# Kernel optimization log

Hardware: AMD Instinct MI355X
Metric: run time of the kernel (lower is better)

## Reference

```python
import jax, jax.numpy as jnp
import numpy as np

K = 5            # kernel_size
MAX_ORIENT = 8
MAX_LEVEL = 4
D = (K - 1) // 2  # pad amount = 2


def setup_inputs() -> dict:
    key = jax.random.key(0)
    k1, k2, k3 = jax.random.split(key, 3)
    x = jax.random.normal(k1, (32, 1, 512, 512), dtype=jnp.float32)
    fwd_f = jax.random.normal(k2, (MAX_ORIENT, 1, K, K), dtype=jnp.float32)
    fwd_f = fwd_f.at[0, 0].set(jnp.ones((K, K), dtype=jnp.float32))  # per __init__
    inv_f = jax.random.normal(k3, (MAX_ORIENT, 1, K, K), dtype=jnp.float32)
    return {"x": x, "forward_filters": fwd_f, "inverse_filters": inv_f}


def _pad_for_tconv(p):
    # faithful port of padding_for_transpose_conv (static python ints)
    ip, op = 0, 0
    if p > 0:
        op = p
    elif p < 0:
        a = -p
        if a % 2 == 0:
            ip = a // 2
        else:
            op = 1
            ip = (a + 1) // 2
    return ip, op


def _conv2d(x, w, stride, pad):
    # torch F.pad(x, (d,d,d,d)) then conv2d(stride) == conv with symmetric padding
    return jax.lax.conv_general_dilated(
        x, w, window_strides=(stride, stride),
        padding=((pad, pad), (pad, pad)),
        dimension_numbers=("NCHW", "OIHW", "NCHW"))


def _conv_transpose2d(x, w, stride, pad, out_pad):
    # torch conv_transpose2d, weight layout (in_ch, out_ch, kH, kW).
    # Equivalent direct conv: flip kernel spatially, swap I/O axes,
    # lhs_dilation=stride, padding lo=k-1-p, hi=k-1-p+output_padding.
    k = w.shape[2]
    w2 = jnp.transpose(jnp.flip(w, (2, 3)), (1, 0, 2, 3))  # OIHW (1,8,5,5)
    padding = tuple((k - 1 - p, k - 1 - p + op) for p, op in zip(pad, out_pad))
    return jax.lax.conv_general_dilated(
        x, w2, window_strides=(1, 1), padding=padding,
        lhs_dilation=(stride, stride),
        dimension_numbers=("NCHW", "OIHW", "NCHW"))


def _forward_transform(x, fwd_f):
    result = [None] * (MAX_LEVEL + 1)
    vimg = x
    level = MAX_LEVEL
    res = None
    while level > 0 and vimg.shape[2] > 1 and vimg.shape[3] > 1:
        res = _conv2d(vimg, fwd_f, 2, D)   # (B, 8, ceil(H/2)+?, ...)
        result[level] = res
        vimg = res[:, :1]                  # lowpass band feeds next level
        level -= 1
    result[0] = res[:, :1]
    return result


def _inverse_transform(coeffs, inp_dim, inv_f):
    rec = coeffs[0]
    for level in range(1, MAX_LEVEL + 1):
        cur = np.array(coeffs[level].shape[2:])
        target = np.array(inp_dim) if level == MAX_LEVEL else np.array(coeffs[level + 1].shape[2:])
        pc = target - 2 * (cur - 1) - K
        ip0, op0 = _pad_for_tconv(int(pc[0]))
        ip1, op1 = _pad_for_tconv(int(pc[1]))
        full = jnp.concatenate([rec, coeffs[level][:, 1:]], axis=1)  # (B,8,h,w)
        rec = _conv_transpose2d(full, inv_f, 2, (ip0, ip1), (op0, op1))
    return rec


def reference(x, forward_filters, inverse_filters):
    coeffs = _forward_transform(x, forward_filters)
    return _inverse_transform(coeffs, x.shape[2:], inverse_filters)
```

## Files before the change

### kernel.cpp

```cpp
#include <hip/hip_runtime.h>

#define NORIENT 8

__device__ __forceinline__ unsigned xcd_swz(unsigned bid, unsigned nwg) {
    unsigned chunk = nwg >> 3;
    return (nwg & 7u) ? bid : (bid & 7u) * chunk + (bid >> 3);
}

__global__ void fwd_conv_kernel(const float* __restrict__ in, long in_img_stride,
                                const float* __restrict__ filt,
                                float* __restrict__ out,
                                int H, int W, int OH, int OW, int N) {
    int OH2 = OH >> 1, OW2 = OW >> 1;
    unsigned sb = xcd_swz(blockIdx.x, gridDim.x);
    long idx = (long)sb * blockDim.x + threadIdx.x;
    long total = (long)N * OH2 * OW2;
    if (idx >= total) return;
    int ox2 = (int)(idx % OW2);
    long t = idx / OW2;
    int oy2 = (int)(t % OH2);
    int n = (int)(t / OH2);

    const float* __restrict__ ip = in + (long)n * in_img_stride;
    int y0 = 4 * oy2 - 2, x0 = 4 * ox2 - 2;

    float patch[7][7];
#pragma unroll
    for (int i = 0; i < 7; ++i) {
        int y = y0 + i;
        bool vy = (y >= 0) & (y < H);
        const float* rowp = ip + (long)(vy ? y : 0) * W;
#pragma unroll
        for (int j = 0; j < 7; ++j) {
            int x = x0 + j;
            bool vx = (x >= 0) & (x < W);
            float v = rowp[vx ? x : 0];
            patch[i][j] = (vy & vx) ? v : 0.f;
        }
    }

    long cs = (long)OH * OW;
    long ob0 = (long)n * NORIENT * cs + (long)(2 * oy2) * OW + 2 * ox2;
#pragma unroll
    for (int c = 0; c < NORIENT; ++c) {
        const float* __restrict__ F = filt + c * 25;
        float a00 = 0.f, a01 = 0.f, a10 = 0.f, a11 = 0.f;
#pragma unroll
        for (int i = 0; i < 5; ++i) {
#pragma unroll
            for (int j = 0; j < 5; ++j) {
                float wv = F[i * 5 + j];
                a00 = fmaf(patch[i][j],         wv, a00);
                a01 = fmaf(patch[i][j + 2],     wv, a01);
                a10 = fmaf(patch[i + 2][j],     wv, a10);
                a11 = fmaf(patch[i + 2][j + 2], wv, a11);
            }
        }
        long ob = ob0 + (long)c * cs;
        *(float2*)&out[ob]      = make_float2(a00, a01);
        *(float2*)&out[ob + OW] = make_float2(a10, a11);
    }
}

__global__ void inv_tconv_kernel(const float* __restrict__ rec, long rec_img_stride,
                                 const float* __restrict__ coef,
                                 const float* __restrict__ filt,
                                 float* __restrict__ out,
                                 int h, int w, int N) {
    int h2 = h >> 1, w2 = w >> 1;
    unsigned sb = xcd_swz(blockIdx.x, gridDim.x);
    long idx = (long)sb * blockDim.x + threadIdx.x;
    long total = (long)N * h2 * w2;
    if (idx >= total) return;
    int b0 = (int)(idx % w2);
    long t = idx / w2;
    int a0 = (int)(t % h2);
    int n = (int)(t / h2);

    const float* __restrict__ rp = rec + (long)n * rec_img_stride;
    const float* __restrict__ cp = coef + (long)n * (long)NORIENT * h * w;
    int cs = h * w;

    bool fmv = a0 > 0, fpv = a0 < h2 - 1;
    bool um = b0 > 0, up = b0 < w2 - 1;
    float fm = fmv ? 1.f : 0.f, fp_ = fpv ? 1.f : 0.f;
    int r0 = (fmv ? 2 * a0 - 1 : 0) * w;
    int r1 = (2 * a0) * w;
    int r2 = (2 * a0 + 1) * w;
    int r3 = (fpv ? 2 * a0 + 2 : 2 * a0 + 1) * w;
    int cL = um ? 2 * b0 - 2 : 0;
    int cM = 2 * b0;
    int cR = up ? 2 * b0 + 2 : 0;

    float acc[2][2][2][2];
#pragma unroll
    for (int i = 0; i < 2; ++i)
#pragma unroll
        for (int j = 0; j < 2; ++j)
#pragma unroll
            for (int k = 0; k < 2; ++k)
#pragma unroll
                for (int l = 0; l < 2; ++l) acc[i][j][k][l] = 0.f;

    auto do_channel = [&](const float* __restrict__ src, const float* __restrict__ F) {
        float P[4][4];
        const int ro[4] = {r0, r1, r2, r3};
        const float rm[4] = {fm, 1.f, 1.f, fp_};
#pragma unroll
        for (int r = 0; r < 4; ++r) {
            const float* base = src + ro[r];
            float2 L = *(const float2*)(base + cL);
            float2 M = *(const float2*)(base + cM);
            float2 R = *(const float2*)(base + cR);
            float mask = rm[r];
            P[r][0] = (um ? L.y : 0.f) * mask;
            P[r][1] = M.x * mask;
            P[r][2] = M.y * mask;
            P[r][3] = (up ? R.x : 0.f) * mask;
        }
#pragma unroll
        for (int a = 0; a < 3; ++a) {
#pragma unroll
            for (int b = 0; b < 3; ++b) {
                float w00 = F[(4 - 2 * a) * 5 + (4 - 2 * b)];
                float w01 = (b >= 1) ? F[(4 - 2 * a) * 5 + (5 - 2 * b)] : 0.f;
                float w10 = (a >= 1) ? F[(5 - 2 * a) * 5 + (4 - 2 * b)] : 0.f;
                float w11 = (a >= 1 && b >= 1) ? F[(5 - 2 * a) * 5 + (5 - 2 * b)] : 0.f;
#pragma unroll
                for (int sr = 0; sr < 2; ++sr) {
#pragma unroll
                    for (int sc = 0; sc < 2; ++sc) {
                        float pv = P[sr + a][sc + b];
                        acc[sr][sc][0][0] = fmaf(pv, w00, acc[sr][sc][0][0]);
                        if (b >= 1) acc[sr][sc][0][1] = fmaf(pv, w01, acc[sr][sc][0][1]);
                        if (a >= 1) acc[sr][sc][1][0] = fmaf(pv, w10, acc[sr][sc][1][0]);
                        if (a >= 1 && b >= 1)
                                    acc[sr][sc][1][1] = fmaf(pv, w11, acc[sr][sc][1][1]);
                    }
                }
            }
        }
    };

    do_channel(rp, filt);
#pragma unroll
    for (int c = 1; c < NORIENT; ++c)
        do_channel(cp + (long)c * cs, filt + c * 25);

    int OW = w << 1;
    long ob = (long)n * 4 * (long)cs + (long)(4 * a0) * OW + 4 * b0;
    *(float4*)(out + ob)          = make_float4(acc[0][0][0][0], acc[0][0][0][1],
                                                acc[0][1][0][0], acc[0][1][0][1]);
    *(float4*)(out + ob + OW)     = make_float4(acc[0][0][1][0], acc[0][0][1][1],
                                                acc[0][1][1][0], acc[0][1][1][1]);
    *(float4*)(out + ob + 2 * OW) = make_float4(acc[1][0][0][0], acc[1][0][0][1],
                                                acc[1][1][0][0], acc[1][1][0][1]);
    *(float4*)(out + ob + 3 * OW) = make_float4(acc[1][0][1][0], acc[1][0][1][1],
                                                acc[1][1][1][0], acc[1][1][1][1]);
}

extern "C" void kernel_launch(void* const* d_in, const int* in_sizes, int n_in,
                              void* d_out, int out_size, void* d_ws, size_t ws_size,
                              hipStream_t stream) {
    const float* x     = (const float*)d_in[0];
    const float* fwd_f = (const float*)d_in[1];
    const float* inv_f = (const float*)d_in[2];
    float* out = (float*)d_out;
    float* ws  = (float*)d_ws;

    const int N = 32;

    float* l4 = ws;
    float* l3 = l4 + 16777216;
    float* l2 = l3 + 4194304;
    float* l1 = l2 + 1048576;
    float* r1 = l1 + 262144;
    float* r2 = r1 + 131072;
    float* r3 = r2 + 524288;

    dim3 blk(256);
    auto nblocks = [](long total) { return dim3((unsigned)((total + 255) / 256)); };

    fwd_conv_kernel<<<nblocks(32L * 128 * 128), blk, 0, stream>>>(
        x, 512L * 512, fwd_f, l4, 512, 512, 256, 256, N);
    fwd_conv_kernel<<<nblocks(32L * 64 * 64), blk, 0, stream>>>(
        l4, 8L * 256 * 256, fwd_f, l3, 256, 256, 128, 128, N);
    fwd_conv_kernel<<<nblocks(32L * 32 * 32), blk, 0, stream>>>(
        l3, 8L * 128 * 128, fwd_f, l2, 128, 128, 64, 64, N);
    fwd_conv_kernel<<<nblocks(32L * 16 * 16), blk, 0, stream>>>(
        l2, 8L * 64 * 64, fwd_f, l1, 64, 64, 32, 32, N);

    inv_tconv_kernel<<<nblocks(32L * 16 * 16), blk, 0, stream>>>(
        l1, 8L * 32 * 32, l1, inv_f, r1, 32, 32, N);
    inv_tconv_kernel<<<nblocks(32L * 32 * 32), blk, 0, stream>>>(
        r1, 64L * 64, l2, inv_f, r2, 64, 64, N);
    inv_tconv_kernel<<<nblocks(32L * 64 * 64), blk, 0, stream>>>(
        r2, 128L * 128, l3, inv_f, r3, 128, 128, N);
    inv_tconv_kernel<<<nblocks(32L * 128 * 128), blk, 0, stream>>>(
        r3, 256L * 256, l4, inv_f, out, 256, 256, N);
}
```

Before: 112.8 us.

## Compute 2x4 output tile per thread in forward conv with float4 row loads

```diff
diff --git a/kernel.cpp b/kernel.cpp
--- a/kernel.cpp
+++ b/kernel.cpp
@@ -11,54 +11,74 @@
                                 const float* __restrict__ filt,
                                 float* __restrict__ out,
                                 int H, int W, int OH, int OW, int N) {
-    int OH2 = OH >> 1, OW2 = OW >> 1;
+    int OHB = OH >> 1, OWB = OW >> 2;
     unsigned sb = xcd_swz(blockIdx.x, gridDim.x);
     long idx = (long)sb * blockDim.x + threadIdx.x;
-    long total = (long)N * OH2 * OW2;
+    long total = (long)N * OHB * OWB;
     if (idx >= total) return;
-    int ox2 = (int)(idx % OW2);
-    long t = idx / OW2;
-    int oy2 = (int)(t % OH2);
-    int n = (int)(t / OH2);
+    int oxb = (int)(idx % OWB);
+    long t = idx / OWB;
+    int oyb = (int)(t % OHB);
+    int n = (int)(t / OHB);
 
     const float* __restrict__ ip = in + (long)n * in_img_stride;
-    int y0 = 4 * oy2 - 2, x0 = 4 * ox2 - 2;
-
-    float patch[7][7];
-#pragma unroll
-    for (int i = 0; i < 7; ++i) {
-        int y = y0 + i;
+    int x0 = 8 * oxb;
+    bool um = oxb > 0, up = (x0 + 8) < W;
+    int bA = um ? x0 - 4 : 0;
+    int bD = up ? x0 + 8 : W - 4;
+
+    float acc[NORIENT][2][4];
+#pragma unroll
+    for (int c = 0; c < NORIENT; ++c)
+#pragma unroll
+        for (int dy = 0; dy < 2; ++dy)
+#pragma unroll
+            for (int dx = 0; dx < 4; ++dx) acc[c][dy][dx] = 0.f;
+
+#pragma unroll
+    for (int r = 0; r < 7; ++r) {
+        int y = 4 * oyb - 2 + r;
         bool vy = (y >= 0) & (y < H);
-        const float* rowp = ip + (long)(vy ? y : 0) * W;
-#pragma unroll
-        for (int j = 0; j < 7; ++j) {
-            int x = x0 + j;
-            bool vx = (x >= 0) & (x < W);
-            float v = rowp[vx ? x : 0];
-            patch[i][j] = (vy & vx) ? v : 0.f;
+        int yc = vy ? y : (y < 0 ? 0 : H - 1);
+        float rm = vy ? 1.f : 0.f;
+        const float* __restrict__ row = ip + (long)yc * W;
+        float4 A = *(const float4*)(row + bA);
+        float4 B = *(const float4*)(row + x0);
+        float4 C = *(const float4*)(row + x0 + 4);
+        float4 D = *(const float4*)(row + bD);
+        float mL = um ? rm : 0.f, mR = up ? rm : 0.f;
+        float P[11];
+        P[0] = A.z * mL; P[1] = A.w * mL;
+        P[2] = B.x * rm; P[3] = B.y * rm; P[4] = B.z * rm; P[5] = B.w * rm;
+        P[6] = C.x * rm; P[7] = C.y * rm; P[8] = C.z * rm; P[9] = C.w * rm;
+        P[10] = D.x * mR;
+
+#pragma unroll
+        for (int dy = 0; dy < 2; ++dy) {
+            int i = r - 2 * dy;
+            if (i < 0 || i > 4) continue;
+#pragma unroll
+            for (int j = 0; j < 5; ++j) {
+#pragma unroll
+                for (int c = 0; c < NORIENT; ++c) {
+                    float wv = filt[c * 25 + i * 5 + j];
+#pragma unroll
+                    for (int dx = 0; dx < 4; ++dx)
+                        acc[c][dy][dx] = fmaf(P[2 * dx + j], wv, acc[c][dy][dx]);
+                }
+            }
         }
     }
 
     long cs = (long)OH * OW;
-    long ob0 = (long)n * NORIENT * cs + (long)(2 * oy2) * OW + 2 * ox2;
+    long ob0 = (long)n * NORIENT * cs + (long)(2 * oyb) * OW + 4 * oxb;
 #pragma unroll
     for (int c = 0; c < NORIENT; ++c) {
-        const float* __restrict__ F = filt + c * 25;
-        float a00 = 0.f, a01 = 0.f, a10 = 0.f, a11 = 0.f;
-#pragma unroll
-        for (int i = 0; i < 5; ++i) {
-#pragma unroll
-            for (int j = 0; j < 5; ++j) {
-                float wv = F[i * 5 + j];
-                a00 = fmaf(patch[i][j],         wv, a00);
-                a01 = fmaf(patch[i][j + 2],     wv, a01);
-                a10 = fmaf(patch[i + 2][j],     wv, a10);
-                a11 = fmaf(patch[i + 2][j + 2], wv, a11);
-            }
-        }
-        long ob = ob0 + (long)c * cs;
-        *(float2*)&out[ob]      = make_float2(a00, a01);
-        *(float2*)&out[ob + OW] = make_float2(a10, a11);
+#pragma unroll
+        for (int dy = 0; dy < 2; ++dy) {
+            *(float4*)(out + ob0 + (long)c * cs + (long)dy * OW) =
+                make_float4(acc[c][dy][0], acc[c][dy][1], acc[c][dy][2], acc[c][dy][3]);
+        }
     }
 }
 
@@ -181,13 +201,13 @@
     dim3 blk(256);
     auto nblocks = [](long total) { return dim3((unsigned)((total + 255) / 256)); };
 
-    fwd_conv_kernel<<<nblocks(32L * 128 * 128), blk, 0, stream>>>(
+    fwd_conv_kernel<<<nblocks(32L * 128 * 64), blk, 0, stream>>>(
         x, 512L * 512, fwd_f, l4, 512, 512, 256, 256, N);
-    fwd_conv_kernel<<<nblocks(32L * 64 * 64), blk, 0, stream>>>(
+    fwd_conv_kernel<<<nblocks(32L * 64 * 32), blk, 0, stream>>>(
         l4, 8L * 256 * 256, fwd_f, l3, 256, 256, 128, 128, N);
-    fwd_conv_kernel<<<nblocks(32L * 32 * 32), blk, 0, stream>>>(
+    fwd_conv_kernel<<<nblocks(32L * 32 * 16), blk, 0, stream>>>(
         l3, 8L * 128 * 128, fwd_f, l2, 128, 128, 64, 64, N);
-    fwd_conv_kernel<<<nblocks(32L * 16 * 16), blk, 0, stream>>>(
+    fwd_conv_kernel<<<nblocks(32L * 16 * 8), blk, 0, stream>>>(
         l2, 8L * 64 * 64, fwd_f, l1, 64, 64, 32, 32, N);
 
     inv_tconv_kernel<<<nblocks(32L * 16 * 16), blk, 0, stream>>>(
```

Result: slower. 175.2 us (+55.3%).

## Rewrite forward conv as LDS-tiled kernel with one wave per orientation

Applied to the files above, without the earlier changes.

```diff
diff --git a/kernel.cpp b/kernel.cpp
--- a/kernel.cpp
+++ b/kernel.cpp
@@ -7,59 +7,86 @@
     return (nwg & 7u) ? bid : (bid & 7u) * chunk + (bid >> 3);
 }
 
-__global__ void fwd_conv_kernel(const float* __restrict__ in, long in_img_stride,
-                                const float* __restrict__ filt,
-                                float* __restrict__ out,
-                                int H, int W, int OH, int OW, int N) {
-    int OH2 = OH >> 1, OW2 = OW >> 1;
+__global__ void fwd_conv_wave_kernel(const float* __restrict__ in, long in_img_stride,
+                                     const float* __restrict__ filt,
+                                     float* __restrict__ out,
+                                     int H, int W, int OH, int OW, int N) {
+    constexpr int SROW = 104;
+    __shared__ float tile[67 * SROW];
+
+    int nbx = OW >> 5, nby = OH >> 5;
     unsigned sb = xcd_swz(blockIdx.x, gridDim.x);
-    long idx = (long)sb * blockDim.x + threadIdx.x;
-    long total = (long)N * OH2 * OW2;
-    if (idx >= total) return;
-    int ox2 = (int)(idx % OW2);
-    long t = idx / OW2;
-    int oy2 = (int)(t % OH2);
-    int n = (int)(t / OH2);
+    int bx = (int)(sb % nbx);
+    unsigned t = sb / nbx;
+    int by = (int)(t % nby);
+    int n = (int)(t / nby);
 
     const float* __restrict__ ip = in + (long)n * in_img_stride;
-    int y0 = 4 * oy2 - 2, x0 = 4 * ox2 - 2;
-
-    float patch[7][7];
-#pragma unroll
-    for (int i = 0; i < 7; ++i) {
-        int y = y0 + i;
-        bool vy = (y >= 0) & (y < H);
-        const float* rowp = ip + (long)(vy ? y : 0) * W;
-#pragma unroll
-        for (int j = 0; j < 7; ++j) {
-            int x = x0 + j;
-            bool vx = (x >= 0) & (x < W);
-            float v = rowp[vx ? x : 0];
-            patch[i][j] = (vy & vx) ? v : 0.f;
+    int tid = threadIdx.x;
+
+    int w = __builtin_amdgcn_readfirstlane(tid >> 6);
+    const float* __restrict__ F = filt + w * 25;
+    float Wt[25];
+#pragma unroll
+    for (int k = 0; k < 25; ++k) Wt[k] = F[k];
+
+    int gy0 = 64 * by - 2, gx0 = 64 * bx - 4;
+#pragma unroll
+    for (int k = 0; k < 3; ++k) {
+        int e = tid + k * 512;
+        if (e < 67 * 18) {
+            int row = e / 18, m = e - row * 18;
+            int gy = gy0 + row, gx = gx0 + 4 * m;
+            bool vl = (gy >= 0) & (gy < H) & (gx >= 0) & (gx <= W - 4);
+            float4 val = *(const float4*)(ip + (vl ? ((long)gy * W + gx) : 0));
+            float msk = vl ? 1.f : 0.f;
+            int off = row * SROW + 4 * m + 4 * (m >> 1);
+            *(float4*)&tile[off] = make_float4(val.x * msk, val.y * msk,
+                                               val.z * msk, val.w * msk);
         }
     }
+    __syncthreads();
+
+    int lane = tid & 63;
+    int lx = lane & 7, ly = lane >> 3;
+
+    float acc[4][4];
+#pragma unroll
+    for (int o = 0; o < 4; ++o)
+#pragma unroll
+        for (int dx = 0; dx < 4; ++dx) acc[o][dx] = 0.f;
+
+#pragma unroll
+    for (int r = 0; r < 11; ++r) {
+        int base = (8 * ly + r) * SROW + 12 * lx;
+        float4 A = *(const float4*)&tile[base];
+        float4 B = *(const float4*)&tile[base + 4];
+        float4 C = *(const float4*)&tile[base + 12];
+        float4 Dd = *(const float4*)&tile[base + 16];
+        float P[16] = {A.x, A.y, A.z, A.w, B.x, B.y, B.z, B.w,
+                       C.x, C.y, C.z, C.w, Dd.x, Dd.y, Dd.z, Dd.w};
+
+#pragma unroll
+        for (int o = 0; o < 4; ++o) {
+            int i = r - 2 * o;
+            if (i < 0 || i > 4) continue;
+#pragma unroll
+            for (int j = 0; j < 5; ++j) {
+                float wv = Wt[i * 5 + j];
+#pragma unroll
+                for (int dx = 0; dx < 4; ++dx)
+                    acc[o][dx] = fmaf(P[2 + 2 * dx + j], wv, acc[o][dx]);
+            }
+        }
+    }
 
     long cs = (long)OH * OW;
-    long ob0 = (long)n * NORIENT * cs + (long)(2 * oy2) * OW + 2 * ox2;
-#pragma unroll
-    for (int c = 0; c < NORIENT; ++c) {
-        const float* __restrict__ F = filt + c * 25;
-        float a00 = 0.f, a01 = 0.f, a10 = 0.f, a11 = 0.f;
-#pragma unroll
-        for (int i = 0; i < 5; ++i) {
-#pragma unroll
-            for (int j = 0; j < 5; ++j) {
-                float wv = F[i * 5 + j];
-                a00 = fmaf(patch[i][j],         wv, a00);
-                a01 = fmaf(patch[i][j + 2],     wv, a01);
-                a10 = fmaf(patch[i + 2][j],     wv, a10);
-                a11 = fmaf(patch[i + 2][j + 2], wv, a11);
-            }
-        }
-        long ob = ob0 + (long)c * cs;
-        *(float2*)&out[ob]      = make_float2(a00, a01);
-        *(float2*)&out[ob + OW] = make_float2(a10, a11);
-    }
+    int oy = 32 * by + 4 * ly, ox = 32 * bx + 4 * lx;
+    long ob = ((long)n * NORIENT + w) * cs + (long)oy * OW + ox;
+#pragma unroll
+    for (int o = 0; o < 4; ++o)
+        *(float4*)(out + ob + (long)o * OW) =
+            make_float4(acc[o][0], acc[o][1], acc[o][2], acc[o][3]);
 }
 
 __global__ void inv_tconv_kernel(const float* __restrict__ rec, long rec_img_stride,
@@ -178,16 +205,16 @@
     float* r2 = r1 + 131072;
     float* r3 = r2 + 524288;
 
-    dim3 blk(256);
+    dim3 blkF(512), blk(256);
     auto nblocks = [](long total) { return dim3((unsigned)((total + 255) / 256)); };
 
-    fwd_conv_kernel<<<nblocks(32L * 128 * 128), blk, 0, stream>>>(
+    fwd_conv_wave_kernel<<<dim3(32 * 8 * 8), blkF, 0, stream>>>(
         x, 512L * 512, fwd_f, l4, 512, 512, 256, 256, N);
-    fwd_conv_kernel<<<nblocks(32L * 64 * 64), blk, 0, stream>>>(
+    fwd_conv_wave_kernel<<<dim3(32 * 4 * 4), blkF, 0, stream>>>(
         l4, 8L * 256 * 256, fwd_f, l3, 256, 256, 128, 128, N);
-    fwd_conv_kernel<<<nblocks(32L * 32 * 32), blk, 0, stream>>>(
+    fwd_conv_wave_kernel<<<dim3(32 * 2 * 2), blkF, 0, stream>>>(
         l3, 8L * 128 * 128, fwd_f, l2, 128, 128, 64, 64, N);
-    fwd_conv_kernel<<<nblocks(32L * 16 * 16), blk, 0, stream>>>(
+    fwd_conv_wave_kernel<<<dim3(32 * 1 * 1), blkF, 0, stream>>>(
         l2, 8L * 64 * 64, fwd_f, l1, 64, 64, 32, 32, N);
 
     inv_tconv_kernel<<<nblocks(32L * 16 * 16), blk, 0, stream>>>(
```

Result: faster. 96.53 us (-14.4%).
